# Kernel tuning notes

Hardware: AMD Instinct MI355X
Metric: run time of the kernel (lower is better)

The kernel has to match this reference:

```python
import jax, jax.numpy as jnp
import numpy as np

T, B, N, N_ATOM = 5, 65536, 16, 51

def setup_inputs() -> dict:
    key = jax.random.key(0)
    ks = jax.random.split(key, 6)
    dist = jax.random.uniform(ks[0], (B, N, N_ATOM), jnp.float32, 0.01, 1.0)
    dist = dist / dist.sum(-1, keepdims=True)          # valid prob dist (>0, sums to 1)
    next_n_dist = jax.random.uniform(ks[1], (B, N, N_ATOM), jnp.float32, 0.01, 1.0)
    next_n_dist = next_n_dist / next_n_dist.sum(-1, keepdims=True)
    action = jax.random.randint(ks[2], (B,), 0, N, dtype=jnp.int32)
    next_n_action = jax.random.randint(ks[3], (B,), 0, N, dtype=jnp.int32)
    reward = jax.random.normal(ks[4], (T, B), dtype=jnp.float32)
    done = jax.random.randint(ks[5], (B,), 0, 2) > 0
    weight = jnp.ones((B,), jnp.float32)
    return dict(dist=dist, next_n_dist=next_n_dist, action=action,
                next_n_action=next_n_action, reward=reward, done=done,
                weight=weight, gamma=jnp.float32(0.99),
                v_min=jnp.float32(-10.0), v_max=jnp.float32(10.0))

def reference(dist, next_n_dist, action, next_n_action, reward, done, weight, gamma, v_min, v_max):
    Bsz, _, n_atom = dist.shape
    nstep = reward.shape[0]
    f32 = jnp.float32
    delta_z = (v_max - v_min) / f32(n_atom - 1)
    support = v_min + delta_z * jnp.arange(n_atom, dtype=f32)        # (n_atom,)
    batch = jnp.arange(Bsz)

    target_dist = next_n_dist[batch, next_n_action]                  # (B, n_atom) gather

    # n-step discounted reward: sum_i gamma^i * reward[i]
    reward_factor = gamma ** jnp.arange(nstep, dtype=f32)            # (T,)
    r = jnp.einsum('t,tb->b', reward_factor, reward)                 # (B,)

    not_done = 1.0 - done.astype(f32)
    target_z = r[:, None] + not_done[:, None] * (gamma ** nstep) * support[None, :]
    target_z = jnp.clip(target_z, v_min, v_max)                      # (B, n_atom)

    b = (target_z - v_min) / delta_z
    l = jnp.floor(b).astype(jnp.int32)
    u = jnp.ceil(b).astype(jnp.int32)
    # fix disappearing mass when l == b == u (sequential, matching torch reference)
    l = l - ((u > 0) & (l == u)).astype(jnp.int32)
    u = u + ((l < n_atom - 1) & (l == u)).astype(jnp.int32)

    # scatter-add histogram projection onto fixed support
    proj = jnp.zeros_like(target_dist)
    proj = proj.at[batch[:, None], l].add(target_dist * (u.astype(f32) - b))
    proj = proj.at[batch[:, None], u].add(target_dist * (b - l.astype(f32)))

    log_p = jnp.log(dist[batch, action])                             # (B, n_atom) gather
    td_err = -(log_p * proj).sum(-1)                                 # (B,)
    loss = (td_err * weight).mean()
    return loss, td_err
```

## Files before the change

kernel.cpp:

```cpp
#include <hip/hip_runtime.h>

#define NSTEP 5
#define NB    65536
#define NACT  16
#define NATOM 51
#define MAIN_BLOCKS 2048
#define THREADS 256

__global__ void detect_done_layout(const unsigned char* __restrict__ db,
                                   int* __restrict__ flag) {
    int t = threadIdx.x;
    unsigned char v = db[1024 * t + 1];
    unsigned long long m = __ballot(v != 0);
    if (t == 0) *flag = (m != 0ULL) ? 1 : 0;
}

__global__ __launch_bounds__(THREADS)
void dist_td_main(const float* __restrict__ dist,
                  const float* __restrict__ next_n_dist,
                  const int*   __restrict__ action,
                  const int*   __restrict__ next_n_action,
                  const float* __restrict__ reward,
                  const unsigned char* __restrict__ done_raw,
                  const float* __restrict__ weight,
                  const float* __restrict__ gamma_p,
                  const float* __restrict__ vmin_p,
                  const float* __restrict__ vmax_p,
                  const int*   __restrict__ flag_p,
                  float* __restrict__ td_out,
                  float* __restrict__ partials)
{
    const int lane = threadIdx.x & 63;
    const int wid  = threadIdx.x >> 6;
    const int wave = blockIdx.x * (THREADS / 64) + wid;
    const int nwaves = MAIN_BLOCKS * (THREADS / 64);

    const float gamma = gamma_p[0];
    const float vmin  = vmin_p[0];
    const float vmax  = vmax_p[0];
    const float dz    = (vmax - vmin) / (float)(NATOM - 1);
    const float inv_dz = 1.0f / dz;
    float g5 = gamma;
    #pragma unroll
    for (int i = 1; i < NSTEP; ++i) g5 *= gamma;
    const int bool_layout = *flag_p;

    const bool  act     = lane < NATOM;
    const float support = vmin + dz * (float)lane;

    float acc = 0.0f;

    for (int b = wave; b < NB; b += nwaves) {
        const int bu = __builtin_amdgcn_readfirstlane(b);
        const int a  = action[bu];
        const int na = next_n_action[bu];

        float r = 0.0f, gf = 1.0f;
        #pragma unroll
        for (int t = 0; t < NSTEP; ++t) { r += gf * reward[t * NB + bu]; gf *= gamma; }

        float nd;
        if (bool_layout) nd = (done_raw[bu] != 0) ? 0.0f : 1.0f;
        else             nd = (((const int*)done_raw)[bu] != 0) ? 0.0f : 1.0f;
        const float w = weight[bu];

        float td = 0.0f, lp = 0.0f;
        if (act) {
            td = next_n_dist[(b * NACT + na) * NATOM + lane];
            lp = __logf(dist[(b * NACT + a) * NATOM + lane]);
        }

        float tz = r + nd * g5 * support;
        tz = fminf(fmaxf(tz, vmin), vmax);
        const float bf = (tz - vmin) * inv_dz;
        int l = (int)floorf(bf);
        int u = (int)ceilf(bf);
        if (u > 0 && l == u) l -= 1;
        if (l < NATOM - 1 && l == u) u += 1;

        const float lp_l = __shfl(lp, l);
        const float lp_u = __shfl(lp, u);
        float contrib = act
            ? -td * (((float)u - bf) * lp_l + (bf - (float)l) * lp_u)
            : 0.0f;

        #pragma unroll
        for (int off = 32; off >= 1; off >>= 1)
            contrib += __shfl_xor(contrib, off);

        if (lane == 0) {
            td_out[b] = contrib;
            acc += contrib * w;
        }
    }

    __shared__ float s_acc[THREADS / 64];
    if (lane == 0) s_acc[wid] = acc;
    __syncthreads();
    if (threadIdx.x == 0) {
        float s = 0.0f;
        #pragma unroll
        for (int i = 0; i < THREADS / 64; ++i) s += s_acc[i];
        partials[blockIdx.x] = s;
    }
}

__global__ void reduce_loss(const float* __restrict__ partials,
                            float* __restrict__ loss) {
    __shared__ float s_acc[4];
    float v = 0.0f;
    for (int i = threadIdx.x; i < MAIN_BLOCKS; i += 256) v += partials[i];
    #pragma unroll
    for (int off = 32; off >= 1; off >>= 1) v += __shfl_xor(v, off);
    const int lane = threadIdx.x & 63, wid = threadIdx.x >> 6;
    if (lane == 0) s_acc[wid] = v;
    __syncthreads();
    if (threadIdx.x == 0)
        loss[0] = (s_acc[0] + s_acc[1] + s_acc[2] + s_acc[3]) * (1.0f / (float)NB);
}

extern "C" void kernel_launch(void* const* d_in, const int* in_sizes, int n_in,
                              void* d_out, int out_size, void* d_ws, size_t ws_size,
                              hipStream_t stream) {
    const float* dist    = (const float*)d_in[0];
    const float* nnd     = (const float*)d_in[1];
    const int*   act     = (const int*)d_in[2];
    const int*   nact    = (const int*)d_in[3];
    const float* reward  = (const float*)d_in[4];
    const unsigned char* done = (const unsigned char*)d_in[5];
    const float* weight  = (const float*)d_in[6];
    const float* gamma   = (const float*)d_in[7];
    const float* vmin    = (const float*)d_in[8];
    const float* vmax    = (const float*)d_in[9];
    float* out = (float*)d_out;

    int*   flag     = (int*)d_ws;
    float* partials = (float*)((char*)d_ws + 256);

    detect_done_layout<<<1, 64, 0, stream>>>(done, flag);
    dist_td_main<<<MAIN_BLOCKS, THREADS, 0, stream>>>(
        dist, nnd, act, nact, reward, done, weight, gamma, vmin, vmax,
        flag, out + 1, partials);
    reduce_loss<<<1, 256, 0, stream>>>(partials, out);
}
```

Measured before the change: 399.2 us.

## Batch eight contiguous samples per wave and hoist all loads ahead of compute

Each wave now handles eight consecutive batch rows instead of grid-striding one row at a time. All per-row scalars and the gathered distribution rows are loaded up front into register arrays, so many independent loads are in flight before any log or shuffle work begins. The grid size is derived from this mapping, and td outputs go out as one contiguous store per wave. Register pressure rises with the unrolled arrays.

```diff
diff --git a/kernel.cpp b/kernel.cpp
--- a/kernel.cpp
+++ b/kernel.cpp
@@ -4,8 +4,10 @@
 #define NB    65536
 #define NACT  16
 #define NATOM 51
-#define MAIN_BLOCKS 2048
 #define THREADS 256
+#define WPB (THREADS / 64)
+#define BPW 8
+#define MAIN_BLOCKS (NB / (WPB * BPW))
 
 __global__ void detect_done_layout(const unsigned char* __restrict__ db,
                                    int* __restrict__ flag) {
@@ -32,13 +34,13 @@
 {
     const int lane = threadIdx.x & 63;
     const int wid  = threadIdx.x >> 6;
-    const int wave = blockIdx.x * (THREADS / 64) + wid;
-    const int nwaves = MAIN_BLOCKS * (THREADS / 64);
+    const int wave = blockIdx.x * WPB + wid;
+    const int b0   = __builtin_amdgcn_readfirstlane(wave * BPW);
 
     const float gamma = gamma_p[0];
     const float vmin  = vmin_p[0];
     const float vmax  = vmax_p[0];
-    const float dz    = (vmax - vmin) / (float)(NATOM - 1);
+    const float dz     = (vmax - vmin) / (float)(NATOM - 1);
     const float inv_dz = 1.0f / dz;
     float g5 = gamma;
     #pragma unroll
@@ -48,29 +50,47 @@
     const bool  act     = lane < NATOM;
     const float support = vmin + dz * (float)lane;
 
-    float acc = 0.0f;
+    int   a[BPW], na[BPW];
+    float r[BPW], nd[BPW], w[BPW], td[BPW], lp[BPW];
 
-    for (int b = wave; b < NB; b += nwaves) {
-        const int bu = __builtin_amdgcn_readfirstlane(b);
-        const int a  = action[bu];
-        const int na = next_n_action[bu];
+    #pragma unroll
+    for (int i = 0; i < BPW; ++i) {
+        a[i]  = action[b0 + i];
+        na[i] = next_n_action[b0 + i];
+        w[i]  = weight[b0 + i];
+        r[i]  = 0.0f;
+    }
+    {
+        float gf = 1.0f;
+        #pragma unroll
+        for (int t = 0; t < NSTEP; ++t) {
+            #pragma unroll
+            for (int i = 0; i < BPW; ++i) r[i] += gf * reward[t * NB + b0 + i];
+            gf *= gamma;
+        }
+    }
+    if (bool_layout) {
+        const unsigned char* p = done_raw + b0;
+        #pragma unroll
+        for (int i = 0; i < BPW; ++i) nd[i] = p[i] ? 0.0f : 1.0f;
+    } else {
+        const int* p = (const int*)done_raw + b0;
+        #pragma unroll
+        for (int i = 0; i < BPW; ++i) nd[i] = p[i] ? 0.0f : 1.0f;
+    }
 
-        float r = 0.0f, gf = 1.0f;
-        #pragma unroll
-        for (int t = 0; t < NSTEP; ++t) { r += gf * reward[t * NB + bu]; gf *= gamma; }
+    #pragma unroll
+    for (int i = 0; i < BPW; ++i) {
+        td[i] = act ? next_n_dist[((b0 + i) * NACT + na[i]) * NATOM + lane] : 0.0f;
+        lp[i] = act ? dist[((b0 + i) * NACT + a[i]) * NATOM + lane] : 1.0f;
+    }
+    #pragma unroll
+    for (int i = 0; i < BPW; ++i) lp[i] = __logf(lp[i]);
 
-        float nd;
-        if (bool_layout) nd = (done_raw[bu] != 0) ? 0.0f : 1.0f;
-        else             nd = (((const int*)done_raw)[bu] != 0) ? 0.0f : 1.0f;
-        const float w = weight[bu];
-
-        float td = 0.0f, lp = 0.0f;
-        if (act) {
-            td = next_n_dist[(b * NACT + na) * NATOM + lane];
-            lp = __logf(dist[(b * NACT + a) * NATOM + lane]);
-        }
-
-        float tz = r + nd * g5 * support;
+    float myout = 0.0f, myloss = 0.0f;
+    #pragma unroll
+    for (int i = 0; i < BPW; ++i) {
+        float tz = r[i] + nd[i] * g5 * support;
         tz = fminf(fmaxf(tz, vmin), vmax);
         const float bf = (tz - vmin) * inv_dz;
         int l = (int)floorf(bf);
@@ -78,31 +98,25 @@
         if (u > 0 && l == u) l -= 1;
         if (l < NATOM - 1 && l == u) u += 1;
 
-        const float lp_l = __shfl(lp, l);
-        const float lp_u = __shfl(lp, u);
-        float contrib = act
-            ? -td * (((float)u - bf) * lp_l + (bf - (float)l) * lp_u)
+        const float lp_l = __shfl(lp[i], l);
+        const float lp_u = __shfl(lp[i], u);
+        float c = act
+            ? -td[i] * (((float)u - bf) * lp_l + (bf - (float)l) * lp_u)
             : 0.0f;
+        #pragma unroll
+        for (int off = 32; off >= 1; off >>= 1) c += __shfl_xor(c, off);
+        if (lane == i) { myout = c; myloss = c * w[i]; }
+    }
+    if (lane < BPW) td_out[b0 + lane] = myout;
 
-        #pragma unroll
-        for (int off = 32; off >= 1; off >>= 1)
-            contrib += __shfl_xor(contrib, off);
+    #pragma unroll
+    for (int off = 4; off >= 1; off >>= 1) myloss += __shfl_xor(myloss, off);
 
-        if (lane == 0) {
-            td_out[b] = contrib;
-            acc += contrib * w;
-        }
-    }
-
-    __shared__ float s_acc[THREADS / 64];
-    if (lane == 0) s_acc[wid] = acc;
+    __shared__ float s_acc[WPB];
+    if (lane == 0) s_acc[wid] = myloss;
     __syncthreads();
-    if (threadIdx.x == 0) {
-        float s = 0.0f;
-        #pragma unroll
-        for (int i = 0; i < THREADS / 64; ++i) s += s_acc[i];
-        partials[blockIdx.x] = s;
-    }
+    if (threadIdx.x == 0)
+        partials[blockIdx.x] = s_acc[0] + s_acc[1] + s_acc[2] + s_acc[3];
 }
 
 __global__ void reduce_loss(const float* __restrict__ partials,
```

Measured after the change: 361.3 us. -9.5%, faster.
